# Kernel optimization log

Hardware: AMD Instinct MI355X
Metric: run time of the kernel (lower is better)

## Reference

```python
import jax, jax.numpy as jnp
import numpy as np
from jax import lax


def conv3x3(x, w):
    # torch Conv2d(k=3, s=1, p=1, bias=False) == cross-correlation, SAME padding
    return lax.conv_general_dilated(x, w, (1, 1), 'SAME',
                                    dimension_numbers=('NCHW', 'OIHW', 'NCHW'))


def pixel_shuffle4(x):
    # (N, C*16, H, W) -> (N, C, 4H, 4W), torch PixelShuffle semantics
    N, C16, H, W = x.shape
    r = 4
    C = C16 // (r * r)
    x = x.reshape(N, C, r, r, H, W)
    x = x.transpose(0, 1, 4, 2, 5, 3)  # N, C, H, r, W, r
    return x.reshape(N, C, H * r, W * r)


def pixel_conv(feat, kernel):
    # feat: (N, 1, H, W); kernel: (N, 25, H, W)
    # torch reference flattens patches with index = c*k*k + kw*k + kh
    # (due to permute(0,2,3,1,5,4)), so kernel channel j -> (kw=j//5, kh=j%5)
    N, C, H, W = feat.shape
    k, pad = 5, 2
    fp = jnp.pad(feat, ((0, 0), (0, 0), (pad, pad), (pad, pad)))
    ker = kernel.reshape(N, k, k, H, W)  # dims: (N, kw, kh, H, W)
    out = jnp.zeros_like(feat)
    for kw in range(k):
        for kh in range(k):
            out = out + fp[:, :, kh:kh + H, kw:kw + W] * ker[:, kw, kh][:, None]
    return out


def setup_inputs() -> dict:
    key = jax.random.key(0)
    ks = jax.random.split(key, 10)

    def w(k, o, i):
        fan_in = i * 9
        return jax.random.normal(k, (o, i, 3, 3), jnp.float32) * np.sqrt(2.0 / fan_in)

    return {
        'x': jax.random.normal(ks[0], (2, 1, 256, 256), jnp.float32),
        'w_e1': w(ks[1], 16, 1),
        'w_e2': w(ks[2], 32, 16),
        'w_e3': w(ks[3], 64, 32),
        'w_d1': w(ks[4], 32, 64),
        'w_d2': w(ks[5], 16, 32),
        'w_k1': w(ks[6], 32, 1),
        'w_k2': w(ks[7], 64, 32),
        'w_k3': w(ks[8], 32, 64),
        'w_k4': w(ks[9], 25, 32),
    }


def reference(x, w_e1, w_e2, w_e3, w_d1, w_d2, w_k1, w_k2, w_k3, w_k4):
    relu = jax.nn.relu
    # encoder
    h = relu(conv3x3(x, w_e1))
    h = relu(conv3x3(h, w_e2))
    h = relu(conv3x3(h, w_e3))
    # decoder
    h = relu(conv3x3(h, w_d1))
    h = relu(conv3x3(h, w_d2))
    # pixel shuffle + relu -> (N, 1, 4H, 4W)
    h = relu(pixel_shuffle4(h))
    # per-pixel kernel prediction branch
    z = relu(conv3x3(h, w_k1))
    z = relu(conv3x3(z, w_k2))
    z = relu(conv3x3(z, w_k3))
    z = relu(conv3x3(z, w_k4))  # (N, 25, 4H, 4W)
    z = pixel_conv(h, z)
    return h + z
```

## Files before the change

### kernel.cpp

```cpp
#include <hip/hip_runtime.h>

template<int CIN, int COUT, int CB, int P, int W>
__global__ __launch_bounds__(256, 4) void conv3x3_relu_k(
    const float* __restrict__ in, const float* __restrict__ wt,
    float* __restrict__ out,
    int in_y0, int in_rows, int out_y0, int out_rows)
{
  static_assert(COUT % CB == 0, "CB must divide COUT");
  constexpr int NCB = COUT / CB;
  constexpr int TW  = 64;
  constexpr int TH  = 4 * P;

  const int n   = blockIdx.z / NCB;
  const int co0 = (blockIdx.z % NCB) * CB;
  const int lx  = threadIdx.x & 63;
  const int yg  = threadIdx.x >> 6;
  const int x0  = blockIdx.x * TW;
  const int x   = x0 + lx;
  const int oy0 = out_y0 + blockIdx.y * TH;
  const int yb  = yg * P;

  const int maxoff = in_rows * W * 4 - 4;

  int   voff[P + 2][3];
  float mrow[P + 2];
#pragma unroll
  for (int r = 0; r < P + 2; ++r) {
    int ry = oy0 + yb + r - 1 - in_y0;
    mrow[r] = (ry >= 0 && ry < in_rows) ? 1.f : 0.f;
    int ryc = ry < 0 ? 0 : (ry >= in_rows ? in_rows - 1 : ry);
    int vo  = (ryc * W + x) * 4;
    voff[r][1] = vo;
    voff[r][0] = (vo > 4 ? vo : 4) - 4;
    int vr = vo + 4;
    voff[r][2] = vr < maxoff ? vr : maxoff;
  }
  const float ml = (x == 0)     ? 0.f : 1.f;
  const float mr = (x == W - 1) ? 0.f : 1.f;

  const bool interior =
      (x0 > 0) && (x0 + TW < W) &&
      ((oy0 - 1 - in_y0) >= 0) && ((oy0 + TH - in_y0) < in_rows);

  float acc[CB][P];
#pragma unroll
  for (int j = 0; j < CB; ++j)
#pragma unroll
    for (int p = 0; p < P; ++p) acc[j][p] = 0.f;

  const float* inN = in + (size_t)n * CIN * in_rows * W;
  const size_t chbytes = (size_t)in_rows * W * 4;

#pragma unroll 1
  for (int ci = 0; ci < CIN; ++ci) {
    const char* bp = (const char*)inN + (size_t)ci * chbytes;

    float va[P + 2][3];
#pragma unroll
    for (int r = 0; r < P + 2; ++r)
#pragma unroll
      for (int c = 0; c < 3; ++c)
        va[r][c] = *(const float*)(bp + voff[r][c]);

    if (!interior) {
#pragma unroll
      for (int r = 0; r < P + 2; ++r) {
#pragma unroll
        for (int c = 0; c < 3; ++c) {
          float m = mrow[r];
          if (c == 0) m *= ml;
          if (c == 2) m *= mr;
          va[r][c] *= m;
        }
      }
    }

#pragma unroll
    for (int j = 0; j < CB; ++j) {
      const float* wp = wt + ((size_t)(co0 + j) * CIN + ci) * 9;
      float w[9];
#pragma unroll
      for (int t = 0; t < 9; ++t) w[t] = wp[t];
#pragma unroll
      for (int t = 0; t < 9; ++t) {
        const int r = t / 3, c = t - r * 3;
#pragma unroll
        for (int p = 0; p < P; ++p)
          acc[j][p] = fmaf(va[p + r][c], w[t], acc[j][p]);
      }
    }
  }

  float* outN = out + (size_t)n * COUT * out_rows * W;
#pragma unroll
  for (int p = 0; p < P; ++p) {
    const int orow = (oy0 + yb + p) - out_y0;
    if (orow < out_rows) {
#pragma unroll
      for (int j = 0; j < CB; ++j) {
        float v = acc[j][p] < 0.f ? 0.f : acc[j][p];
        outN[((size_t)(co0 + j) * out_rows + orow) * W + x] = v;
      }
    }
  }
}

__global__ __launch_bounds__(256) void pixel_shuffle_relu_k(
    const float* __restrict__ in, float* __restrict__ out)
{
  int i = blockIdx.x * 256 + threadIdx.x;
  int n = i >> 20;
  int p = i & 1048575;
  int x = p & 1023, y = p >> 10;
  int c = (y & 3) * 4 + (x & 3);
  float v = in[((size_t)(n * 16 + c) * 256 + (y >> 2)) * 256 + (x >> 2)];
  out[i] = v < 0.f ? 0.f : v;
}

__global__ __launch_bounds__(256) void pixel_conv_add_k(
    const float* __restrict__ h,
    const float* __restrict__ ker,
    float* __restrict__ out,
    int ky0, int krows)
{
  const int tx = threadIdx.x & 15, ty = threadIdx.x >> 4;
  const int x0 = blockIdx.x * 16;
  const int y0 = ky0 + blockIdx.y * 16;

  __shared__ float tile[20][21];
  for (int t = threadIdx.x; t < 20 * 20; t += 256) {
    int r = t / 20, c = t - r * 20;
    int yy = y0 + r - 2, xx = x0 + c - 2;
    float v = 0.f;
    if (yy >= 0 && yy < 1024 && xx >= 0 && xx < 1024) v = h[(size_t)yy * 1024 + xx];
    tile[r][c] = v;
  }
  __syncthreads();

  const int x = x0 + tx, y = y0 + ty;
  float acc = tile[ty + 2][tx + 2];
  const size_t kpix = (size_t)(y - ky0) * 1024 + x;
#pragma unroll
  for (int kw = 0; kw < 5; ++kw) {
#pragma unroll
    for (int kh = 0; kh < 5; ++kh) {
      float kv = ker[(size_t)(kw * 5 + kh) * krows * 1024 + kpix];
      acc = fmaf(tile[ty + kh][tx + kw], kv, acc);
    }
  }
  out[(size_t)y * 1024 + x] = acc;
}

extern "C" void kernel_launch(void* const* d_in, const int* in_sizes, int n_in,
                              void* d_out, int out_size, void* d_ws, size_t ws_size,
                              hipStream_t stream) {
  const float* x    = (const float*)d_in[0];
  const float* w_e1 = (const float*)d_in[1];
  const float* w_e2 = (const float*)d_in[2];
  const float* w_e3 = (const float*)d_in[3];
  const float* w_d1 = (const float*)d_in[4];
  const float* w_d2 = (const float*)d_in[5];
  const float* w_k1 = (const float*)d_in[6];
  const float* w_k2 = (const float*)d_in[7];
  const float* w_k3 = (const float*)d_in[8];
  const float* w_k4 = (const float*)d_in[9];

  const size_t HS_SZ = 8388608;
  const size_t AMIN  = 16777216;
  const size_t BMIN  = 33554432;

  int S = 64;
  {
    const int cand[5] = {1024, 512, 256, 128, 64};
    for (int i = 0; i < 5; ++i) {
      int s = cand[i];
      size_t a = 32ull * (size_t)(s + 6) * 1024 * 4; if (a < AMIN) a = AMIN;
      size_t b = 64ull * (size_t)(s + 4) * 1024 * 4; if (b < BMIN) b = BMIN;
      if (HS_SZ + a + b <= ws_size) { S = s; break; }
    }
  }
  size_t A_SZ = 32ull * (size_t)(S + 6) * 1024 * 4; if (A_SZ < AMIN) A_SZ = AMIN;

  char* ws = (char*)d_ws;
  float* Hs = (float*)(ws);
  float* A  = (float*)(ws + HS_SZ);
  float* B  = (float*)(ws + HS_SZ + A_SZ);
  float* outp = (float*)d_out;

  dim3 blk(256);

  conv3x3_relu_k<1, 16, 16, 2, 256><<<dim3(4, 32, 2), blk, 0, stream>>>(x, w_e1, B, 0, 256, 0, 256);
  conv3x3_relu_k<16, 32, 32, 2, 256><<<dim3(4, 32, 2), blk, 0, stream>>>(B, w_e2, A, 0, 256, 0, 256);
  conv3x3_relu_k<32, 64, 32, 2, 256><<<dim3(4, 32, 4), blk, 0, stream>>>(A, w_e3, B, 0, 256, 0, 256);
  conv3x3_relu_k<64, 32, 32, 2, 256><<<dim3(4, 32, 2), blk, 0, stream>>>(B, w_d1, A, 0, 256, 0, 256);
  conv3x3_relu_k<32, 16, 16, 2, 256><<<dim3(4, 32, 2), blk, 0, stream>>>(A, w_d2, B, 0, 256, 0, 256);
  pixel_shuffle_relu_k<<<dim3(8192), blk, 0, stream>>>(B, Hs);

  const int nstr = 1024 / S;
  for (int n = 0; n < 2; ++n) {
    const float* himg = Hs + (size_t)n * 1048576;
    float* outn = outp + (size_t)n * 1048576;
    for (int s = 0; s < nstr; ++s) {
      const int r0 = s * S, r1 = r0 + S;
      const int z1y0 = (r0 - 3 > 0) ? r0 - 3 : 0;
      const int z1r  = ((r1 + 3 < 1024) ? r1 + 3 : 1024) - z1y0;
      const int z2y0 = (r0 - 2 > 0) ? r0 - 2 : 0;
      const int z2r  = ((r1 + 2 < 1024) ? r1 + 2 : 1024) - z2y0;
      const int z3y0 = (r0 - 1 > 0) ? r0 - 1 : 0;
      const int z3r  = ((r1 + 1 < 1024) ? r1 + 1 : 1024) - z3y0;
      const int g1 = (z1r + 7) / 8, g2 = (z2r + 7) / 8, g3 = (z3r + 7) / 8;

      conv3x3_relu_k<1, 32, 32, 2, 1024><<<dim3(16, g1, 1), blk, 0, stream>>>(
          himg, w_k1, A, 0, 1024, z1y0, z1r);
      conv3x3_relu_k<32, 64, 32, 2, 1024><<<dim3(16, g2, 2), blk, 0, stream>>>(
          A, w_k2, B, z1y0, z1r, z2y0, z2r);
      conv3x3_relu_k<64, 32, 32, 2, 1024><<<dim3(16, g3, 1), blk, 0, stream>>>(
          B, w_k3, A, z2y0, z2r, z3y0, z3r);
      conv3x3_relu_k<32, 25, 25, 2, 1024><<<dim3(16, S / 8, 1), blk, 0, stream>>>(
          A, w_k4, B, z3y0, z3r, r0, S);
      pixel_conv_add_k<<<dim3(64, S / 16), blk, 0, stream>>>(
          himg, B, outn, r0, S);
    }
  }
}
```

Before: 3.312 ms.

## Double-buffer input tap loads and retile convs to 4 rows, 16 channels

The input-channel loop now prefetches the next channel's 3x3 taps into a second register buffer while the current channel is computed, so global load latency is hidden behind FMAs. Most conv launches also move from 2 output rows and 32 channels per thread to 4 rows and 16 channels, with grids adjusted to match. The taller tile reuses each loaded input row across more outputs and halves the work per channel group. The cost is more registers for the two tap buffers, which under launch_bounds(256,4) may cause spills or lower occupancy.

```diff
diff --git a/kernel.cpp b/kernel.cpp
--- a/kernel.cpp
+++ b/kernel.cpp
@@ -51,45 +51,58 @@
   const float* inN = in + (size_t)n * CIN * in_rows * W;
   const size_t chbytes = (size_t)in_rows * W * 4;
 
+  float pfA[P + 2][3], pfB[P + 2][3];
+
+#define LOADTAPS(dst, cidx)                                                  \
+  {                                                                          \
+    const char* bp = (const char*)inN + (size_t)(cidx) * chbytes;            \
+    _Pragma("unroll")                                                        \
+    for (int r = 0; r < P + 2; ++r)                                          \
+      _Pragma("unroll")                                                      \
+      for (int c = 0; c < 3; ++c)                                            \
+        dst[r][c] = *(const float*)(bp + voff[r][c]);                        \
+  }
+
+#define COMPUTE(src, cidx)                                                   \
+  {                                                                          \
+    if (!interior) {                                                         \
+      _Pragma("unroll")                                                      \
+      for (int r = 0; r < P + 2; ++r) {                                      \
+        _Pragma("unroll")                                                    \
+        for (int c = 0; c < 3; ++c) {                                        \
+          float m = mrow[r];                                                 \
+          if (c == 0) m *= ml;                                               \
+          if (c == 2) m *= mr;                                               \
+          src[r][c] *= m;                                                    \
+        }                                                                    \
+      }                                                                      \
+    }                                                                        \
+    _Pragma("unroll")                                                        \
+    for (int j = 0; j < CB; ++j) {                                           \
+      const float* wp = wt + ((size_t)(co0 + j) * CIN + (cidx)) * 9;         \
+      float w[9];                                                            \
+      _Pragma("unroll")                                                      \
+      for (int t = 0; t < 9; ++t) w[t] = wp[t];                              \
+      _Pragma("unroll")                                                      \
+      for (int t = 0; t < 9; ++t) {                                          \
+        const int r = t / 3, c = t - r * 3;                                  \
+        _Pragma("unroll")                                                    \
+        for (int p = 0; p < P; ++p)                                          \
+          acc[j][p] = fmaf(src[p + r][c], w[t], acc[j][p]);                  \
+      }                                                                      \
+    }                                                                        \
+  }
+
+  LOADTAPS(pfA, 0);
 #pragma unroll 1
-  for (int ci = 0; ci < CIN; ++ci) {
-    const char* bp = (const char*)inN + (size_t)ci * chbytes;
-
-    float va[P + 2][3];
-#pragma unroll
-    for (int r = 0; r < P + 2; ++r)
-#pragma unroll
-      for (int c = 0; c < 3; ++c)
-        va[r][c] = *(const float*)(bp + voff[r][c]);
-
-    if (!interior) {
-#pragma unroll
-      for (int r = 0; r < P + 2; ++r) {
-#pragma unroll
-        for (int c = 0; c < 3; ++c) {
-          float m = mrow[r];
-          if (c == 0) m *= ml;
-          if (c == 2) m *= mr;
-          va[r][c] *= m;
-        }
-      }
-    }
-
-#pragma unroll
-    for (int j = 0; j < CB; ++j) {
-      const float* wp = wt + ((size_t)(co0 + j) * CIN + ci) * 9;
-      float w[9];
-#pragma unroll
-      for (int t = 0; t < 9; ++t) w[t] = wp[t];
-#pragma unroll
-      for (int t = 0; t < 9; ++t) {
-        const int r = t / 3, c = t - r * 3;
-#pragma unroll
-        for (int p = 0; p < P; ++p)
-          acc[j][p] = fmaf(va[p + r][c], w[t], acc[j][p]);
-      }
-    }
-  }
+  for (int ci = 0; ci < CIN; ci += 2) {
+    if (ci + 1 < CIN) LOADTAPS(pfB, ci + 1);
+    COMPUTE(pfA, ci);
+    if (ci + 2 < CIN) LOADTAPS(pfA, ci + 2);
+    if (ci + 1 < CIN) COMPUTE(pfB, ci + 1);
+  }
+#undef LOADTAPS
+#undef COMPUTE
 
   float* outN = out + (size_t)n * COUT * out_rows * W;
 #pragma unroll
@@ -189,11 +202,11 @@
 
   dim3 blk(256);
 
-  conv3x3_relu_k<1, 16, 16, 2, 256><<<dim3(4, 32, 2), blk, 0, stream>>>(x, w_e1, B, 0, 256, 0, 256);
-  conv3x3_relu_k<16, 32, 32, 2, 256><<<dim3(4, 32, 2), blk, 0, stream>>>(B, w_e2, A, 0, 256, 0, 256);
-  conv3x3_relu_k<32, 64, 32, 2, 256><<<dim3(4, 32, 4), blk, 0, stream>>>(A, w_e3, B, 0, 256, 0, 256);
-  conv3x3_relu_k<64, 32, 32, 2, 256><<<dim3(4, 32, 2), blk, 0, stream>>>(B, w_d1, A, 0, 256, 0, 256);
-  conv3x3_relu_k<32, 16, 16, 2, 256><<<dim3(4, 32, 2), blk, 0, stream>>>(A, w_d2, B, 0, 256, 0, 256);
+  conv3x3_relu_k<1, 16, 16, 4, 256><<<dim3(4, 16, 2), blk, 0, stream>>>(x, w_e1, B, 0, 256, 0, 256);
+  conv3x3_relu_k<16, 32, 16, 4, 256><<<dim3(4, 16, 4), blk, 0, stream>>>(B, w_e2, A, 0, 256, 0, 256);
+  conv3x3_relu_k<32, 64, 16, 4, 256><<<dim3(4, 16, 8), blk, 0, stream>>>(A, w_e3, B, 0, 256, 0, 256);
+  conv3x3_relu_k<64, 32, 16, 4, 256><<<dim3(4, 16, 4), blk, 0, stream>>>(B, w_d1, A, 0, 256, 0, 256);
+  conv3x3_relu_k<32, 16, 16, 4, 256><<<dim3(4, 16, 2), blk, 0, stream>>>(A, w_d2, B, 0, 256, 0, 256);
   pixel_shuffle_relu_k<<<dim3(8192), blk, 0, stream>>>(B, Hs);
 
   const int nstr = 1024 / S;
@@ -208,13 +221,13 @@
       const int z2r  = ((r1 + 2 < 1024) ? r1 + 2 : 1024) - z2y0;
       const int z3y0 = (r0 - 1 > 0) ? r0 - 1 : 0;
       const int z3r  = ((r1 + 1 < 1024) ? r1 + 1 : 1024) - z3y0;
-      const int g1 = (z1r + 7) / 8, g2 = (z2r + 7) / 8, g3 = (z3r + 7) / 8;
-
-      conv3x3_relu_k<1, 32, 32, 2, 1024><<<dim3(16, g1, 1), blk, 0, stream>>>(
+      const int g1 = (z1r + 15) / 16, g2 = (z2r + 15) / 16, g3 = (z3r + 15) / 16;
+
+      conv3x3_relu_k<1, 32, 16, 4, 1024><<<dim3(16, g1, 2), blk, 0, stream>>>(
           himg, w_k1, A, 0, 1024, z1y0, z1r);
-      conv3x3_relu_k<32, 64, 32, 2, 1024><<<dim3(16, g2, 2), blk, 0, stream>>>(
+      conv3x3_relu_k<32, 64, 16, 4, 1024><<<dim3(16, g2, 4), blk, 0, stream>>>(
           A, w_k2, B, z1y0, z1r, z2y0, z2r);
-      conv3x3_relu_k<64, 32, 32, 2, 1024><<<dim3(16, g3, 1), blk, 0, stream>>>(
+      conv3x3_relu_k<64, 32, 16, 4, 1024><<<dim3(16, g3, 2), blk, 0, stream>>>(
           B, w_k3, A, z2y0, z2r, z3y0, z3r);
       conv3x3_relu_k<32, 25, 25, 2, 1024><<<dim3(16, S / 8, 1), blk, 0, stream>>>(
           A, w_k4, B, z3y0, z3r, r0, S);
```

Result: slower. 9.061 ms (+173.5%).

## Fuse final kernel-prediction conv with pixel conv and repack weights per block

Applied to the files above, without the earlier changes.

Merges the last 32->25 convolution with the per-pixel 5x5 kernel application, so the 25-channel kernel map stays in registers and is never written to or read back from global memory. The input h tile is staged in shared memory for the pixel conv. Weights are repacked once per call into a [block][ci][cb][9] layout, so each block's weights for one input channel are contiguous. Occupancy hint drops from 4 to 2 blocks per CU to leave room for more registers, which could reduce latency hiding.

```diff
diff --git a/kernel.cpp b/kernel.cpp
--- a/kernel.cpp
+++ b/kernel.cpp
@@ -1,7 +1,29 @@
 #include <hip/hip_runtime.h>
 
+
+struct WRepArgs {
+  const float* src[9];
+  float*       dst[9];
+  int cout[9], cin[9], cb[9];
+};
+
+__global__ __launch_bounds__(256) void repack_wts_k(WRepArgs a) {
+  const int L = blockIdx.y;
+  const int cin = a.cin[L], cout = a.cout[L], cb = a.cb[L];
+  const int n = cout * cin * 9;
+  const float* s = a.src[L];
+  float* d = a.dst[L];
+  for (int i = blockIdx.x * 256 + threadIdx.x; i < n; i += gridDim.x * 256) {
+    int co  = i / (cin * 9);
+    int rem = i - co * (cin * 9);
+    int ci  = rem / 9;
+    int t   = rem - ci * 9;
+    d[(((size_t)(co / cb) * cin + ci) * cb + (co % cb)) * 9 + t] = s[i];
+  }
+}
+
 template<int CIN, int COUT, int CB, int P, int W>
-__global__ __launch_bounds__(256, 4) void conv3x3_relu_k(
+__global__ __launch_bounds__(256, 2) void conv3x3_relu_k(
     const float* __restrict__ in, const float* __restrict__ wt,
     float* __restrict__ out,
     int in_y0, int in_rows, int out_y0, int out_rows)
@@ -12,7 +34,8 @@
   constexpr int TH  = 4 * P;
 
   const int n   = blockIdx.z / NCB;
-  const int co0 = (blockIdx.z % NCB) * CB;
+  const int nb  = blockIdx.z % NCB;
+  const int co0 = nb * CB;
   const int lx  = threadIdx.x & 63;
   const int yg  = threadIdx.x >> 6;
   const int x0  = blockIdx.x * TW;
@@ -48,12 +71,14 @@
 #pragma unroll
     for (int p = 0; p < P; ++p) acc[j][p] = 0.f;
 
-  const float* inN = in + (size_t)n * CIN * in_rows * W;
+  const float* inN   = in + (size_t)n * CIN * in_rows * W;
   const size_t chbytes = (size_t)in_rows * W * 4;
+  const float* wbase = wt + (size_t)nb * CIN * CB * 9;
 
 #pragma unroll 1
   for (int ci = 0; ci < CIN; ++ci) {
-    const char* bp = (const char*)inN + (size_t)ci * chbytes;
+    const char*  bp  = (const char*)inN + (size_t)ci * chbytes;
+    const float* wci = wbase + (size_t)ci * CB * 9;
 
     float va[P + 2][3];
 #pragma unroll
@@ -77,7 +102,7 @@
 
 #pragma unroll
     for (int j = 0; j < CB; ++j) {
-      const float* wp = wt + ((size_t)(co0 + j) * CIN + ci) * 9;
+      const float* wp = wci + j * 9;
       float w[9];
 #pragma unroll
       for (int t = 0; t < 9; ++t) w[t] = wp[t];
@@ -102,6 +127,119 @@
         outN[((size_t)(co0 + j) * out_rows + orow) * W + x] = v;
       }
     }
+  }
+}
+
+template<int CIN, int P>
+__global__ __launch_bounds__(256, 2) void conv_k4_pixconv_k(
+    const float* __restrict__ in, const float* __restrict__ wt,
+    const float* __restrict__ h, float* __restrict__ out,
+    int in_y0, int in_rows, int out_y0)
+{
+  constexpr int CB = 25;
+  constexpr int TW = 64, TH = 4 * P, W = 1024;
+
+  const int lx  = threadIdx.x & 63;
+  const int yg  = threadIdx.x >> 6;
+  const int x0  = blockIdx.x * TW;
+  const int x   = x0 + lx;
+  const int oy0 = out_y0 + blockIdx.y * TH;
+  const int yb  = yg * P;
+
+  __shared__ float htile[TH + 4][TW + 4];
+  for (int t = threadIdx.x; t < (TH + 4) * (TW + 4); t += 256) {
+    int r = t / (TW + 4), c = t - r * (TW + 4);
+    int yy = oy0 + r - 2, xx = x0 + c - 2;
+    float v = 0.f;
+    if (yy >= 0 && yy < 1024 && xx >= 0 && xx < W) v = h[(size_t)yy * W + xx];
+    htile[r][c] = v;
+  }
+  __syncthreads();
+
+  const int maxoff = in_rows * W * 4 - 4;
+
+  int   voff[P + 2][3];
+  float mrow[P + 2];
+#pragma unroll
+  for (int r = 0; r < P + 2; ++r) {
+    int ry = oy0 + yb + r - 1 - in_y0;
+    mrow[r] = (ry >= 0 && ry < in_rows) ? 1.f : 0.f;
+    int ryc = ry < 0 ? 0 : (ry >= in_rows ? in_rows - 1 : ry);
+    int vo  = (ryc * W + x) * 4;
+    voff[r][1] = vo;
+    voff[r][0] = (vo > 4 ? vo : 4) - 4;
+    int vr = vo + 4;
+    voff[r][2] = vr < maxoff ? vr : maxoff;
+  }
+  const float ml = (x == 0)     ? 0.f : 1.f;
+  const float mr = (x == W - 1) ? 0.f : 1.f;
+
+  const bool interior =
+      (x0 > 0) && (x0 + TW < W) &&
+      ((oy0 - 1 - in_y0) >= 0) && ((oy0 + TH - in_y0) < in_rows);
+
+  float acc[CB][P];
+#pragma unroll
+  for (int j = 0; j < CB; ++j)
+#pragma unroll
+    for (int p = 0; p < P; ++p) acc[j][p] = 0.f;
+
+  const size_t chbytes = (size_t)in_rows * W * 4;
+
+#pragma unroll 1
+  for (int ci = 0; ci < CIN; ++ci) {
+    const char*  bp  = (const char*)in + (size_t)ci * chbytes;
+    const float* wci = wt + (size_t)ci * CB * 9;
+
+    float va[P + 2][3];
+#pragma unroll
+    for (int r = 0; r < P + 2; ++r)
+#pragma unroll
+      for (int c = 0; c < 3; ++c)
+        va[r][c] = *(const float*)(bp + voff[r][c]);
+
+    if (!interior) {
+#pragma unroll
+      for (int r = 0; r < P + 2; ++r) {
+#pragma unroll
+        for (int c = 0; c < 3; ++c) {
+          float m = mrow[r];
+          if (c == 0) m *= ml;
+          if (c == 2) m *= mr;
+          va[r][c] *= m;
+        }
+      }
+    }
+
+#pragma unroll
+    for (int j = 0; j < CB; ++j) {
+      const float* wp = wci + j * 9;
+      float w[9];
+#pragma unroll
+      for (int t = 0; t < 9; ++t) w[t] = wp[t];
+#pragma unroll
+      for (int t = 0; t < 9; ++t) {
+        const int r = t / 3, c = t - r * 3;
+#pragma unroll
+        for (int p = 0; p < P; ++p)
+          acc[j][p] = fmaf(va[p + r][c], w[t], acc[j][p]);
+      }
+    }
+  }
+
+#pragma unroll
+  for (int p = 0; p < P; ++p) {
+    float a = htile[yb + p + 2][lx + 2];
+#pragma unroll
+    for (int kw = 0; kw < 5; ++kw) {
+#pragma unroll
+      for (int kh = 0; kh < 5; ++kh) {
+        float kv = acc[kw * 5 + kh][p];
+        kv = kv < 0.f ? 0.f : kv;
+        a = fmaf(htile[yb + p + kh][lx + kw], kv, a);
+      }
+    }
+    out[(size_t)(oy0 + yb + p) * W + x] = a;
   }
 }
 
@@ -117,57 +255,23 @@
   out[i] = v < 0.f ? 0.f : v;
 }
 
-__global__ __launch_bounds__(256) void pixel_conv_add_k(
-    const float* __restrict__ h,
-    const float* __restrict__ ker,
-    float* __restrict__ out,
-    int ky0, int krows)
-{
-  const int tx = threadIdx.x & 15, ty = threadIdx.x >> 4;
-  const int x0 = blockIdx.x * 16;
-  const int y0 = ky0 + blockIdx.y * 16;
-
-  __shared__ float tile[20][21];
-  for (int t = threadIdx.x; t < 20 * 20; t += 256) {
-    int r = t / 20, c = t - r * 20;
-    int yy = y0 + r - 2, xx = x0 + c - 2;
-    float v = 0.f;
-    if (yy >= 0 && yy < 1024 && xx >= 0 && xx < 1024) v = h[(size_t)yy * 1024 + xx];
-    tile[r][c] = v;
-  }
-  __syncthreads();
-
-  const int x = x0 + tx, y = y0 + ty;
-  float acc = tile[ty + 2][tx + 2];
-  const size_t kpix = (size_t)(y - ky0) * 1024 + x;
-#pragma unroll
-  for (int kw = 0; kw < 5; ++kw) {
-#pragma unroll
-    for (int kh = 0; kh < 5; ++kh) {
-      float kv = ker[(size_t)(kw * 5 + kh) * krows * 1024 + kpix];
-      acc = fmaf(tile[ty + kh][tx + kw], kv, acc);
-    }
-  }
-  out[(size_t)y * 1024 + x] = acc;
-}
-
 extern "C" void kernel_launch(void* const* d_in, const int* in_sizes, int n_in,
                               void* d_out, int out_size, void* d_ws, size_t ws_size,
                               hipStream_t stream) {
   const float* x    = (const float*)d_in[0];
-  const float* w_e1 = (const float*)d_in[1];
-  const float* w_e2 = (const float*)d_in[2];
-  const float* w_e3 = (const float*)d_in[3];
-  const float* w_d1 = (const float*)d_in[4];
-  const float* w_d2 = (const float*)d_in[5];
-  const float* w_k1 = (const float*)d_in[6];
-  const float* w_k2 = (const float*)d_in[7];
-  const float* w_k3 = (const float*)d_in[8];
-  const float* w_k4 = (const float*)d_in[9];
-
-  const size_t HS_SZ = 8388608;
-  const size_t AMIN  = 16777216;
-  const size_t BMIN  = 33554432;
+  const float* w[9] = { (const float*)d_in[1], (const float*)d_in[2],
+                        (const float*)d_in[3], (const float*)d_in[4],
+                        (const float*)d_in[5], (const float*)d_in[6],
+                        (const float*)d_in[7], (const float*)d_in[8],
+                        (const float*)d_in[9] };
+  const int LCO[9] = {16, 32, 64, 32, 16, 32, 64, 32, 25};
+  const int LCI[9] = { 1, 16, 32, 64, 32,  1, 32, 64, 32};
+  const int LCB[9] = {16, 32, 32, 32, 16, 32, 32, 32, 25};
+
+  const size_t HS_SZ   = 8388608;
+  const size_t WREP_SZ = 524288;
+  const size_t AMIN    = 16777216;
+  const size_t BMIN    = 33554432;
 
   int S = 64;
   {
@@ -176,24 +280,37 @@
       int s = cand[i];
       size_t a = 32ull * (size_t)(s + 6) * 1024 * 4; if (a < AMIN) a = AMIN;
       size_t b = 64ull * (size_t)(s + 4) * 1024 * 4; if (b < BMIN) b = BMIN;
-      if (HS_SZ + a + b <= ws_size) { S = s; break; }
+      if (HS_SZ + WREP_SZ + a + b <= ws_size) { S = s; break; }
     }
   }
   size_t A_SZ = 32ull * (size_t)(S + 6) * 1024 * 4; if (A_SZ < AMIN) A_SZ = AMIN;
 
   char* ws = (char*)d_ws;
-  float* Hs = (float*)(ws);
-  float* A  = (float*)(ws + HS_SZ);
-  float* B  = (float*)(ws + HS_SZ + A_SZ);
+  float* Hs   = (float*)(ws);
+  float* WREP = (float*)(ws + HS_SZ);
+  float* A    = (float*)(ws + HS_SZ + WREP_SZ);
+  float* B    = (float*)(ws + HS_SZ + WREP_SZ + A_SZ);
   float* outp = (float*)d_out;
 
+  WRepArgs ra;
+  float* wr[9];
+  {
+    size_t off = 0;
+    for (int L = 0; L < 9; ++L) {
+      wr[L] = WREP + off;
+      ra.src[L] = w[L]; ra.dst[L] = wr[L];
+      ra.cout[L] = LCO[L]; ra.cin[L] = LCI[L]; ra.cb[L] = LCB[L];
+      off += (size_t)LCO[L] * LCI[L] * 9;
+    }
+  }
   dim3 blk(256);
-
-  conv3x3_relu_k<1, 16, 16, 2, 256><<<dim3(4, 32, 2), blk, 0, stream>>>(x, w_e1, B, 0, 256, 0, 256);
-  conv3x3_relu_k<16, 32, 32, 2, 256><<<dim3(4, 32, 2), blk, 0, stream>>>(B, w_e2, A, 0, 256, 0, 256);
-  conv3x3_relu_k<32, 64, 32, 2, 256><<<dim3(4, 32, 4), blk, 0, stream>>>(A, w_e3, B, 0, 256, 0, 256);
-  conv3x3_relu_k<64, 32, 32, 2, 256><<<dim3(4, 32, 2), blk, 0, stream>>>(B, w_d1, A, 0, 256, 0, 256);
-  conv3x3_relu_k<32, 16, 16, 2, 256><<<dim3(4, 32, 2), blk, 0, stream>>>(A, w_d2, B, 0, 256, 0, 256);
+  repack_wts_k<<<dim3(8, 9), blk, 0, stream>>>(ra);
+
+  conv3x3_relu_k<1, 16, 16, 2, 256><<<dim3(4, 32, 2), blk, 0, stream>>>(x, wr[0], B, 0, 256, 0, 256);
+  conv3x3_relu_k<16, 32, 32, 2, 256><<<dim3(4, 32, 2), blk, 0, stream>>>(B, wr[1], A, 0, 256, 0, 256);
+  conv3x3_relu_k<32, 64, 32, 2, 256><<<dim3(4, 32, 4), blk, 0, stream>>>(A, wr[2], B, 0, 256, 0, 256);
+  conv3x3_relu_k<64, 32, 32, 2, 256><<<dim3(4, 32, 2), blk, 0, stream>>>(B, wr[3], A, 0, 256, 0, 256);
+  conv3x3_relu_k<32, 16, 16, 2, 256><<<dim3(4, 32, 2), blk, 0, stream>>>(A, wr[4], B, 0, 256, 0, 256);
   pixel_shuffle_relu_k<<<dim3(8192), blk, 0, stream>>>(B, Hs);
 
   const int nstr = 1024 / S;
@@ -211,15 +328,13 @@
       const int g1 = (z1r + 7) / 8, g2 = (z2r + 7) / 8, g3 = (z3r + 7) / 8;
 
       conv3x3_relu_k<1, 32, 32, 2, 1024><<<dim3(16, g1, 1), blk, 0, stream>>>(
-          himg, w_k1, A, 0, 1024, z1y0, z1r);
+          himg, wr[5], A, 0, 1024, z1y0, z1r);
       conv3x3_relu_k<32, 64, 32, 2, 1024><<<dim3(16, g2, 2), blk, 0, stream>>>(
-          A, w_k2, B, z1y0, z1r, z2y0, z2r);
+          A, wr[6], B, z1y0, z1r, z2y0, z2r);
       conv3x3_relu_k<64, 32, 32, 2, 1024><<<dim3(16, g3, 1), blk, 0, stream>>>(
-          B, w_k3, A, z2y0, z2r, z3y0, z3r);
-      conv3x3_relu_k<32, 25, 25, 2, 1024><<<dim3(16, S / 8, 1), blk, 0, stream>>>(
-          A, w_k4, B, z3y0, z3r, r0, S);
-      pixel_conv_add_k<<<dim3(64, S / 16), blk, 0, stream>>>(
-          himg, B, outn, r0, S);
-    }
-  }
-}
+          B, wr[7], A, z2y0, z2r, z3y0, z3r);
+      conv_k4_pixconv_k<32, 2><<<dim3(16, S / 8, 1), blk, 0, stream>>>(
+          A, wr[8], himg, outn, z3y0, z3r, r0);
+    }
+  }
+}
```

Measured after the change: 5.375 ms. +62.3%, slower.
